# Kernel optimization log

Measured on AMD Instinct MI355X. Metric: run time of the kernel, lower is better.

The kernel has to match this reference:

```python
import jax, jax.numpy as jnp
import numpy as np

B, SQ, SK, D, H = 4, 2048, 2048, 1024, 16
EPS = 1e-6  # flax LayerNorm default


def layer_norm(x, g, b):
    m = x.mean(-1, keepdims=True)
    var = ((x - m) ** 2).mean(-1, keepdims=True)
    return (x - m) * jax.lax.rsqrt(var + EPS) * g + b


def setup_inputs() -> dict:
    key = jax.random.key(0)
    ks = jax.random.split(key, 16)
    s = 1.0 / np.sqrt(D).astype(np.float32)
    inp = {
        'q': jax.random.normal(ks[0], (B, SQ, D), jnp.float32),
        'k': jax.random.normal(ks[1], (B, SK, D), jnp.float32),
        'v': jax.random.normal(ks[2], (B, SK, D), jnp.float32),
        'mask': jax.random.randint(ks[3], (B, SK), 0, 2).astype(bool),
        'Wq': jax.random.normal(ks[4], (D, D), jnp.float32) * s,
        'bq': jnp.zeros((D,), jnp.float32),
        'Wk': jax.random.normal(ks[5], (D, D), jnp.float32) * s,
        'bk': jnp.zeros((D,), jnp.float32),
        'Wv': jax.random.normal(ks[6], (D, D), jnp.float32) * s,
        'bv': jnp.zeros((D,), jnp.float32),
        'Wo': jax.random.normal(ks[7], (D, D), jnp.float32) * s,
        'bo': jnp.zeros((D,), jnp.float32),
        'g1': jnp.ones((D,), jnp.float32),
        'b1': jnp.zeros((D,), jnp.float32),
        'g2': jnp.ones((D,), jnp.float32),
        'b2': jnp.zeros((D,), jnp.float32),
    }
    return inp


def reference(q, k, v, mask, Wq, bq, Wk, bk, Wv, bv, Wo, bo, g1, b1, g2, b2):
    qp = q @ Wq + bq                      # [B, SQ, D]
    kp = k @ Wk + bk                      # [B, SK, D]
    vp = v @ Wv + bv
    qh = qp.reshape(B, SQ, H, D // H)     # head = slice of last dim (matches scatter)
    kh = kp.reshape(B, SK, H, D // H)
    vh = vp.reshape(B, SK, H, D // H)
    # NOTE: original scales by sqrt(dim_out) (full dim), not head dim
    logits = jnp.einsum('bqhd,bkhd->bhqk', qh, kh) / np.sqrt(D).astype(np.float32)
    m = mask[:, None, None, :]            # [B,1,1,SK] broadcast over heads & queries
    A = jax.nn.softmax(jnp.where(m, logits, -jnp.inf), axis=-1)
    A = jnp.where(jnp.isnan(A), 0.0, A)   # fully-masked rows -> 0 (as in original)
    attn = jnp.einsum('bhqk,bkhd->bqhd', A, vh).reshape(B, SQ, D)  # gather heads
    x = layer_norm(qp + attn, g1, b1)
    out = layer_norm(x + jax.nn.relu(x @ Wo + bo), g2, b2)
    return out
```

## Files before the change

kernel.cpp:

```cpp
#include <hip/hip_runtime.h>

#define B_   4
#define SQS  2048
#define SKS  2048
#define DM   1024
#define H_   16
#define MT   8192

typedef __attribute__((ext_vector_type(8))) short bf16x8;
typedef __attribute__((ext_vector_type(4))) float f32x4;

__device__ __forceinline__ float bf2f(unsigned int u) { return __uint_as_float(u << 16); }
__device__ __forceinline__ unsigned short f2bf(float f) {
  unsigned int u = __float_as_uint(f);
  return (unsigned short)((u + 0x7fffu + ((u >> 16) & 1u)) >> 16);
}
__device__ __forceinline__ unsigned int pk_bf16(float a, float b) {
  return __builtin_amdgcn_perm(__float_as_uint(b) + 0x8000u,
                               __float_as_uint(a) + 0x8000u, 0x07060302u);
}
__device__ __forceinline__ unsigned int pk_trunc(float a, float b) {
  return __builtin_amdgcn_perm(__float_as_uint(b), __float_as_uint(a), 0x07060302u);
}
__device__ __forceinline__ float fexp2(float x) {
#if __has_builtin(__builtin_amdgcn_exp2f)
  return __builtin_amdgcn_exp2f(x);
#else
  return __expf(x * 0.69314718056f);
#endif
}
__device__ __forceinline__ void async16(const void* g, void* l) {
  __builtin_amdgcn_global_load_lds((const __attribute__((address_space(1))) unsigned int*)g,
                                   (__attribute__((address_space(3))) unsigned int*)l,
                                   16, 0, 0);
}

#define KSCALE 0.0450842200f
#define BIAS_UNMASKED 0.0028151213f

__global__ __launch_bounds__(256)
void prep_all(const float* __restrict__ q, const float* __restrict__ k,
              const float* __restrict__ v, const int* __restrict__ mask,
              const float* __restrict__ Wq, const float* __restrict__ Wk,
              const float* __restrict__ Wv, const float* __restrict__ Wo,
              unsigned short* __restrict__ qi, unsigned short* __restrict__ ki,
              unsigned short* __restrict__ vi,
              unsigned short* __restrict__ Wqt, unsigned short* __restrict__ Wkt,
              unsigned short* __restrict__ Wvt, unsigned short* __restrict__ Wot,
              float* __restrict__ mskb)
{
  __shared__ float s[32][33];
  const int bx = blockIdx.x, tid = threadIdx.x;
  if (bx < 24576) {
    const int which = bx >> 13, i = bx & 8191;
    const float* src = (which == 0) ? q : (which == 1) ? k : v;
    unsigned short* dst = (which == 0) ? qi : (which == 1) ? ki : vi;
    size_t o = ((size_t)i * 256 + tid) * 4;
    float4 f = *(const float4*)(src + o);
    uint2 u;
    u.x = pk_bf16(f.x, f.y);
    u.y = pk_bf16(f.z, f.w);
    *(uint2*)(dst + o) = u;
  } else if (bx < 28672) {
    const int idx = bx - 24576;
    const int w = idx >> 10, t = idx & 1023;
    const int n0 = (t & 31) * 32, k0 = (t >> 5) * 32;
    const float* W = (w == 0) ? Wq : (w == 1) ? Wk : (w == 2) ? Wv : Wo;
    unsigned short* Wt = (w == 0) ? Wqt : (w == 1) ? Wkt : (w == 2) ? Wvt : Wot;
#pragma unroll
    for (int p = 0; p < 4; p++) {
      int c = p * 256 + tid;
      int r = c >> 5, cc = c & 31;
      s[r][cc] = W[(size_t)(k0 + r) * DM + n0 + cc];
    }
    __syncthreads();
#pragma unroll
    for (int p = 0; p < 4; p++) {
      int c = p * 256 + tid;
      int r = c >> 5, cc = c & 31;
      Wt[(size_t)(n0 + r) * DM + k0 + cc] = f2bf(s[cc][r]);
    }
  } else {
    int i = (bx - 28672) * 256 + tid;
    mskb[i] = mask[i] ? BIAS_UNMASKED : -1e30f;
  }
}

__global__ __launch_bounds__(256)
void qkv_gemm(const unsigned short* __restrict__ A0, const unsigned short* __restrict__ A1,
              const unsigned short* __restrict__ A2,
              const unsigned short* __restrict__ W0, const unsigned short* __restrict__ W1,
              const unsigned short* __restrict__ W2,
              const float* __restrict__ s0, const float* __restrict__ s1,
              const float* __restrict__ s2,
              unsigned short* __restrict__ o0, unsigned short* __restrict__ o1,
              unsigned short* __restrict__ vT)
{
  const int L = blockIdx.x + (blockIdx.y << 3) + (blockIdx.z << 9);
  const int g = L & 7, i5 = L >> 3;
  const int nblk = i5 & 7;
  const int yz = (i5 >> 3) + g * 24;
  const int mblk = yz & 63;
  const int z = yz >> 6;

  const unsigned short* A  = (z == 0) ? A0 : (z == 1) ? A1 : A2;
  const unsigned short* Wt = (z == 0) ? W0 : (z == 1) ? W1 : W2;
  const float* bias        = (z == 0) ? s0 : (z == 1) ? s1 : s2;

  __shared__ short As[128 * 64];
  __shared__ short Bs[128 * 64];
  const int tid = threadIdx.x;
  const int m0 = mblk * 128, n0 = nblk * 128;
  const int wave = tid >> 6, ln = tid & 15, qd = (tid & 63) >> 4;
  const int wm = (wave >> 1) * 64, wn = (wave & 1) * 64;

  int srow[4], sgj[4];
#pragma unroll
  for (int u = 0; u < 4; u++) {
    int c = u * 256 + tid;
    srow[u] = c >> 3;
    sgj[u] = ((c & 7) ^ (srow[u] & 7)) * 8;
  }

  f32x4 acc[4][4];
  const f32x4 vzero = {0.f, 0.f, 0.f, 0.f};
#pragma unroll
  for (int i = 0; i < 4; i++)
#pragma unroll
    for (int j = 0; j < 4; j++) acc[i][j] = vzero;

  for (int k0 = 0; k0 < DM; k0 += 64) {
    __syncthreads();
#pragma unroll
    for (int u = 0; u < 4; u++) {
      int c = u * 256 + tid;
      async16(A  + (size_t)(m0 + srow[u]) * DM + k0 + sgj[u], (char*)As + c * 16);
      async16(Wt + (size_t)(n0 + srow[u]) * DM + k0 + sgj[u], (char*)Bs + c * 16);
    }
    __syncthreads();

#pragma unroll
    for (int kk = 0; kk < 2; kk++) {
      const int ch = ((kk * 4 + qd) ^ (ln & 7)) * 8;
      bf16x8 af[4], bfr[4];
#pragma unroll
      for (int i = 0; i < 4; i++)
        af[i] = *(const bf16x8*)(As + (wm + i * 16 + ln) * 64 + ch);
#pragma unroll
      for (int j = 0; j < 4; j++)
        bfr[j] = *(const bf16x8*)(Bs + (wn + j * 16 + ln) * 64 + ch);
#pragma unroll
      for (int i = 0; i < 4; i++)
#pragma unroll
        for (int j = 0; j < 4; j++)
          acc[i][j] = __builtin_amdgcn_mfma_f32_16x16x32_bf16(af[i], bfr[j], acc[i][j], 0, 0, 0);
    }
  }

  if (z != 2) {
    unsigned short* C = (z == 0) ? o0 : o1;
    const float sc = (z == 1) ? KSCALE : 1.0f;
#pragma unroll
    for (int j = 0; j < 4; j++) {
      int col = n0 + wn + j * 16 + ln;
      float bj = bias[col];
#pragma unroll
      for (int i = 0; i < 4; i++) {
        int row = m0 + wm + i * 16 + qd * 4;
#pragma unroll
        for (int r = 0; r < 4; r++)
          C[(size_t)(row + r) * DM + col] = f2bf((acc[i][j][r] + bj) * sc);
      }
    }
  } else {
#pragma unroll
    for (int j = 0; j < 4; j++) {
      int col = n0 + wn + j * 16 + ln;
      int h = col >> 6, d = col & 63;
      float bj = bias[col];
#pragma unroll
      for (int i = 0; i < 4; i++) {
        int tok0 = m0 + wm + i * 16 + qd * 4;
        int bb = tok0 >> 11;
        int kcol = ((tok0 & 2047) & ~63) + (i & 1) * 32 + qd * 8 + ((i >> 1) & 1) * 4;
        uint2 u;
        u.x = pk_bf16(acc[i][j][0] + bj, acc[i][j][1] + bj);
        u.y = pk_bf16(acc[i][j][2] + bj, acc[i][j][3] + bj);
        *(uint2*)(vT + ((size_t)(bb * H_ + h) * 64 + d) * SKS + kcol) = u;
      }
    }
  }
}

__global__ __launch_bounds__(256)
void gemm_bf16(const unsigned short* __restrict__ A,
               const unsigned short* __restrict__ Wt,
               const float* __restrict__ bias,
               unsigned short* __restrict__ C,
               int relu)
{
  const int L = blockIdx.x + (blockIdx.y << 3);
  const int g = L & 7, i5 = L >> 3;
  const int nblk = i5 & 7;
  const int mblk = (i5 >> 3) + (g << 3);

  __shared__ short As[128 * 64];
  __shared__ short Bs[128 * 64];
  const int tid = threadIdx.x;
  const int m0 = mblk * 128, n0 = nblk * 128;
  const int wave = tid >> 6, ln = tid & 15, qd = (tid & 63) >> 4;
  const int wm = (wave >> 1) * 64, wn = (wave & 1) * 64;

  int srow[4], sgj[4];
#pragma unroll
  for (int u = 0; u < 4; u++) {
    int c = u * 256 + tid;
    srow[u] = c >> 3;
    sgj[u] = ((c & 7) ^ (srow[u] & 7)) * 8;
  }

  f32x4 acc[4][4];
  const f32x4 vzero = {0.f, 0.f, 0.f, 0.f};
#pragma unroll
  for (int i = 0; i < 4; i++)
#pragma unroll
    for (int j = 0; j < 4; j++) acc[i][j] = vzero;

  for (int k0 = 0; k0 < DM; k0 += 64) {
    __syncthreads();
#pragma unroll
    for (int u = 0; u < 4; u++) {
      int c = u * 256 + tid;
      async16(A  + (size_t)(m0 + srow[u]) * DM + k0 + sgj[u], (char*)As + c * 16);
      async16(Wt + (size_t)(n0 + srow[u]) * DM + k0 + sgj[u], (char*)Bs + c * 16);
    }
    __syncthreads();

#pragma unroll
    for (int kk = 0; kk < 2; kk++) {
      const int ch = ((kk * 4 + qd) ^ (ln & 7)) * 8;
      bf16x8 af[4], bfr[4];
#pragma unroll
      for (int i = 0; i < 4; i++)
        af[i] = *(const bf16x8*)(As + (wm + i * 16 + ln) * 64 + ch);
#pragma unroll
      for (int j = 0; j < 4; j++)
        bfr[j] = *(const bf16x8*)(Bs + (wn + j * 16 + ln) * 64 + ch);
#pragma unroll
      for (int i = 0; i < 4; i++)
#pragma unroll
        for (int j = 0; j < 4; j++)
          acc[i][j] = __builtin_amdgcn_mfma_f32_16x16x32_bf16(af[i], bfr[j], acc[i][j], 0, 0, 0);
    }
  }

#pragma unroll
  for (int j = 0; j < 4; j++) {
    int col = n0 + wn + j * 16 + ln;
    float bj = bias[col];
#pragma unroll
    for (int i = 0; i < 4; i++) {
      int row = m0 + wm + i * 16 + qd * 4;
#pragma unroll
      for (int r = 0; r < 4; r++) {
        float v = acc[i][j][r] + bj;
        if (relu) v = fmaxf(v, 0.f);
        C[(size_t)(row + r) * DM + col] = f2bf(v);
      }
    }
  }
}

__global__ __launch_bounds__(256, 2)
void attn_fwd(const unsigned short* __restrict__ qp,
              const unsigned short* __restrict__ kp,
              const unsigned short* __restrict__ vT,
              const float* __restrict__ maskb,
              unsigned short* __restrict__ O0,
              unsigned short* __restrict__ O1,
              float* __restrict__ lws)
{
  __shared__ short Ks[128 * 64];
  __shared__ short Vs[64 * 128];
  __shared__ float bias_s[128];

  const int tid = threadIdx.x;
  const int L = blockIdx.x + (blockIdx.y << 4) + (blockIdx.z << 8);
  const int g = L & 7, i5 = L >> 3;
  const int half = i5 & 1;
  const int qblk = (i5 >> 1) & 7;
  const int bh = (i5 >> 4) + (g << 3);
  const int h = bh & 15, b = bh >> 4;
  const int q0 = qblk * 256;
  const int koff0 = half * (SKS / 2);
  const int wave = tid >> 6, ln = tid & 15, qd = (tid & 63) >> 4;

  int kRow[4], kOff[4], vRow[4], vOff[4];
#pragma unroll
  for (int u = 0; u < 4; u++) {
    int c = u * 256 + tid;
    kRow[u] = c >> 3;
    kOff[u] = ((c & 7) ^ (kRow[u] & 7)) * 8;
    vRow[u] = c >> 4;
    int j = c & 15;
    vOff[u] = ((j & 8) | ((j ^ vRow[u]) & 7)) * 8;
  }

  const unsigned short* kbase = kp + (size_t)(b * SKS) * DM + (h << 6);
  const unsigned short* vbase = vT + (size_t)((b * H_ + h) * 64) * SKS;

  bf16x8 qf[4][2];
#pragma unroll
  for (int gq = 0; gq < 4; gq++) {
    const unsigned short* qrow =
        qp + (size_t)(b * SQS + q0 + wave * 64 + gq * 16 + ln) * DM + (h << 6);
    qf[gq][0] = *(const bf16x8*)(qrow + qd * 8);
    qf[gq][1] = *(const bf16x8*)(qrow + 32 + qd * 8);
  }

  union { bf16x8 v; unsigned int u[4]; } onesf;
  onesf.u[0] = onesf.u[1] = onesf.u[2] = onesf.u[3] = 0x3F803F80u;

  const f32x4 vzero = {0.f, 0.f, 0.f, 0.f};
  f32x4 oA[4][4], lacc[4];
#pragma unroll
  for (int gq = 0; gq < 4; gq++) {
    lacc[gq] = vzero;
#pragma unroll
    for (int t = 0; t < 4; t++) oA[gq][t] = vzero;
  }

  for (int kt = 0; kt < SKS / 2 / 128; kt++) {
    const int k0 = koff0 + kt * 128;
    __syncthreads();
    if (tid < 128) bias_s[tid] = maskb[b * SKS + k0 + tid];
#pragma unroll
    for (int u = 0; u < 4; u++) {
      int c = u * 256 + tid;
      async16(kbase + (size_t)(k0 + kRow[u]) * DM + kOff[u], (char*)Ks + c * 16);
      async16(vbase + (size_t)vRow[u] * SKS + k0 + vOff[u], (char*)Vs + c * 16);
    }
    __syncthreads();

#pragma unroll
    for (int h2 = 0; h2 < 2; h2++) {
      bf16x8 kf[4][2];
      f32x4 btv[4];
#pragma unroll
      for (int t = 0; t < 4; t++) {
        const short* krow = Ks + (h2 * 64 + t * 16 + ln) * 64;
        kf[t][0] = *(const bf16x8*)(krow + ((0 + qd) ^ (ln & 7)) * 8);
        kf[t][1] = *(const bf16x8*)(krow + ((4 + qd) ^ (ln & 7)) * 8);
        btv[t] = *(const f32x4*)(bias_s + h2 * 64 + t * 16 + qd * 4);
      }

      bf16x8 pf[4][2];
#pragma unroll
      for (int gq = 0; gq < 4; gq++) {
        f32x4 sS[4];
#pragma unroll
        for (int t = 0; t < 4; t++) {
          f32x4 a = __builtin_amdgcn_mfma_f32_16x16x32_bf16(kf[t][0], qf[gq][0], btv[t], 0, 0, 0);
          sS[t]   = __builtin_amdgcn_mfma_f32_16x16x32_bf16(kf[t][1], qf[gq][1], a,      0, 0, 0);
        }
        float p[4][4];
#pragma unroll
        for (int t = 0; t < 4; t++) {
          p[t][0] = fexp2(sS[t][0]);
          p[t][1] = fexp2(sS[t][1]);
          p[t][2] = fexp2(sS[t][2]);
          p[t][3] = fexp2(sS[t][3]);
        }
        union { bf16x8 v; unsigned int u[4]; } P0, P1;
        P0.u[0] = pk_trunc(p[0][0], p[0][1]);
        P0.u[1] = pk_trunc(p[0][2], p[0][3]);
        P0.u[2] = pk_trunc(p[2][0], p[2][1]);
        P0.u[3] = pk_trunc(p[2][2], p[2][3]);
        P1.u[0] = pk_trunc(p[1][0], p[1][1]);
        P1.u[1] = pk_trunc(p[1][2], p[1][3]);
        P1.u[2] = pk_trunc(p[3][0], p[3][1]);
        P1.u[3] = pk_trunc(p[3][2], p[3][3]);
        pf[gq][0] = P0.v;
        pf[gq][1] = P1.v;
        lacc[gq] = __builtin_amdgcn_mfma_f32_16x16x32_bf16(pf[gq][0], onesf.v, lacc[gq], 0, 0, 0);
        lacc[gq] = __builtin_amdgcn_mfma_f32_16x16x32_bf16(pf[gq][1], onesf.v, lacc[gq], 0, 0, 0);
      }

#pragma unroll
      for (int t2 = 0; t2 < 4; t2++) {
        const short* vrow = Vs + (t2 * 16 + ln) * 128;
        bf16x8 vf0 = *(const bf16x8*)(vrow + (h2 * 8 + ((0 + qd) ^ (ln & 7))) * 8);
        bf16x8 vf1 = *(const bf16x8*)(vrow + (h2 * 8 + ((4 + qd) ^ (ln & 7))) * 8);
#pragma unroll
        for (int gq = 0; gq < 4; gq++) {
          oA[gq][t2] = __builtin_amdgcn_mfma_f32_16x16x32_bf16(pf[gq][0], vf0, oA[gq][t2], 0, 0, 0);
          oA[gq][t2] = __builtin_amdgcn_mfma_f32_16x16x32_bf16(pf[gq][1], vf1, oA[gq][t2], 0, 0, 0);
        }
      }
    }
  }

  unsigned short* obuf = half ? O1 : O0;
  float* lbuf = lws + (size_t)half * (B_ * H_ * SQS);
#pragma unroll
  for (int gq = 0; gq < 4; gq++) {
    int qloc = q0 + wave * 64 + gq * 16 + qd * 4;
    if (ln == 0) {
#pragma unroll
      for (int r = 0; r < 4; r++)
        lbuf[(size_t)(b * H_ + h) * SQS + qloc + r] = lacc[gq][r];
    }
#pragma unroll
    for (int t2 = 0; t2 < 4; t2++)
#pragma unroll
      for (int r = 0; r < 4; r++) {
        size_t idx = (size_t)(b * SQS + qloc + r) * DM + (h << 6) + t2 * 16 + ln;
        obuf[idx] = f2bf(oA[gq][t2][r]);
      }
  }
}

__global__ __launch_bounds__(256)
void ln_merge(const unsigned short* __restrict__ Xa, const unsigned short* __restrict__ O0,
              const unsigned short* __restrict__ O1, const float* __restrict__ lws,
              const float* __restrict__ gamma, const float* __restrict__ beta,
              unsigned short* __restrict__ outb)
{
  const int row = blockIdx.x, tid = threadIdx.x;
  const int b = row >> 11, q = row & 2047;
  const int h = tid >> 4;
  const size_t lidx = (size_t)(b * H_ + h) * SQS + q;
  float la = lws[lidx], lb2 = lws[lidx + (size_t)(B_ * H_ * SQS)];
  float lsum = la + lb2;
  float linv = (lsum > 0.f) ? 1.0f / lsum : 0.f;

  const size_t base = (size_t)row * DM + tid * 4;
  uint2 ua = *(const uint2*)(Xa + base);
  uint2 u0 = *(const uint2*)(O0 + base);
  uint2 u1 = *(const uint2*)(O1 + base);
  float v0 = bf2f(ua.x & 0xffffu) + (bf2f(u0.x & 0xffffu) + bf2f(u1.x & 0xffffu)) * linv;
  float v1 = bf2f(ua.x >> 16)     + (bf2f(u0.x >> 16)     + bf2f(u1.x >> 16))     * linv;
  float v2 = bf2f(ua.y & 0xffffu) + (bf2f(u0.y & 0xffffu) + bf2f(u1.y & 0xffffu)) * linv;
  float v3 = bf2f(ua.y >> 16)     + (bf2f(u0.y >> 16)     + bf2f(u1.y >> 16))     * linv;

  float s  = (v0 + v1) + (v2 + v3);
  float s2 = (v0 * v0 + v1 * v1) + (v2 * v2 + v3 * v3);
#pragma unroll
  for (int off = 1; off < 64; off <<= 1) {
    s  += __shfl_xor(s, off);
    s2 += __shfl_xor(s2, off);
  }
  __shared__ float red[8];
  if ((tid & 63) == 0) { red[tid >> 6] = s; red[4 + (tid >> 6)] = s2; }
  __syncthreads();
  float S  = (red[0] + red[1]) + (red[2] + red[3]);
  float S2 = (red[4] + red[5]) + (red[6] + red[7]);
  float mean = S * (1.0f / 1024.0f);
  float var  = S2 * (1.0f / 1024.0f) - mean * mean;
  float rstd = rsqrtf(var + 1e-6f);
  int c = tid * 4;
  float o0 = (v0 - mean) * rstd * gamma[c + 0] + beta[c + 0];
  float o1 = (v1 - mean) * rstd * gamma[c + 1] + beta[c + 1];
  float o2 = (v2 - mean) * rstd * gamma[c + 2] + beta[c + 2];
  float o3 = (v3 - mean) * rstd * gamma[c + 3] + beta[c + 3];
  uint2 o;
  o.x = pk_bf16(o0, o1);
  o.y = pk_bf16(o2, o3);
  *(uint2*)(outb + base) = o;
}

__global__ __launch_bounds__(256)
void ln_fuse(const unsigned short* __restrict__ Xa, const unsigned short* __restrict__ Xb,
             const float* __restrict__ gamma, const float* __restrict__ beta,
             float* __restrict__ outf)
{
  const int row = blockIdx.x, tid = threadIdx.x;
  const size_t base = (size_t)row * DM + tid * 4;
  uint2 ua = *(const uint2*)(Xa + base);
  uint2 ub = *(const uint2*)(Xb + base);
  float v0 = bf2f(ua.x & 0xffffu) + bf2f(ub.x & 0xffffu);
  float v1 = bf2f(ua.x >> 16)     + bf2f(ub.x >> 16);
  float v2 = bf2f(ua.y & 0xffffu) + bf2f(ub.y & 0xffffu);
  float v3 = bf2f(ua.y >> 16)     + bf2f(ub.y >> 16);
  float s  = (v0 + v1) + (v2 + v3);
  float s2 = (v0 * v0 + v1 * v1) + (v2 * v2 + v3 * v3);
#pragma unroll
  for (int off = 1; off < 64; off <<= 1) {
    s  += __shfl_xor(s, off);
    s2 += __shfl_xor(s2, off);
  }
  __shared__ float red[8];
  if ((tid & 63) == 0) { red[tid >> 6] = s; red[4 + (tid >> 6)] = s2; }
  __syncthreads();
  float S  = (red[0] + red[1]) + (red[2] + red[3]);
  float S2 = (red[4] + red[5]) + (red[6] + red[7]);
  float mean = S * (1.0f / 1024.0f);
  float var  = S2 * (1.0f / 1024.0f) - mean * mean;
  float rstd = rsqrtf(var + 1e-6f);
  int c = tid * 4;
  float o0 = (v0 - mean) * rstd * gamma[c + 0] + beta[c + 0];
  float o1 = (v1 - mean) * rstd * gamma[c + 1] + beta[c + 1];
  float o2 = (v2 - mean) * rstd * gamma[c + 2] + beta[c + 2];
  float o3 = (v3 - mean) * rstd * gamma[c + 3] + beta[c + 3];
  float4 o = {o0, o1, o2, o3};
  *(float4*)(outf + base) = o;
}

extern "C" void kernel_launch(void* const* d_in, const int* in_sizes, int n_in,
                              void* d_out, int out_size, void* d_ws, size_t ws_size,
                              hipStream_t stream)
{
  (void)in_sizes; (void)n_in; (void)out_size; (void)ws_size;
  const float* q    = (const float*)d_in[0];
  const float* k    = (const float*)d_in[1];
  const float* v    = (const float*)d_in[2];
  const int*   mask = (const int*)  d_in[3];
  const float* Wq   = (const float*)d_in[4];
  const float* bq   = (const float*)d_in[5];
  const float* Wk   = (const float*)d_in[6];
  const float* bk   = (const float*)d_in[7];
  const float* Wv   = (const float*)d_in[8];
  const float* bv   = (const float*)d_in[9];
  const float* Wo   = (const float*)d_in[10];
  const float* bo   = (const float*)d_in[11];
  const float* g1   = (const float*)d_in[12];
  const float* b1   = (const float*)d_in[13];
  const float* g2   = (const float*)d_in[14];
  const float* b2   = (const float*)d_in[15];

  char* ws = (char*)d_ws;
  const size_t SZ16 = (size_t)16 << 20;
  unsigned short* qi   = (unsigned short*)(ws + 0 * SZ16);
  unsigned short* ki   = (unsigned short*)(ws + 1 * SZ16);
  unsigned short* vi   = (unsigned short*)(ws + 2 * SZ16);
  unsigned short* qpb  = (unsigned short*)(ws + 3 * SZ16);
  unsigned short* kpb  = (unsigned short*)(ws + 4 * SZ16);
  unsigned short* vTb  = (unsigned short*)(ws + 6 * SZ16);
  unsigned short* Wqt  = (unsigned short*)(ws + 7 * SZ16 + ((size_t)0 << 20));
  unsigned short* Wkt  = (unsigned short*)(ws + 7 * SZ16 + ((size_t)2 << 20));
  unsigned short* Wvt  = (unsigned short*)(ws + 7 * SZ16 + ((size_t)4 << 20));
  unsigned short* Wot  = (unsigned short*)(ws + 7 * SZ16 + ((size_t)6 << 20));
  float*          mskb = (float*)         (ws + 7 * SZ16 + ((size_t)8 << 20));
  float*          lws  = (float*)         (ws + 7 * SZ16 + ((size_t)9 << 20));
  unsigned short* O0b  = qi;
  unsigned short* O1b  = vi;
  unsigned short* xb   = ki;
  unsigned short* hb   = vTb;

  prep_all     <<<28704,            256, 0, stream>>>(q, k, v, mask, Wq, Wk, Wv, Wo,
                                                      qi, ki, vi, Wqt, Wkt, Wvt, Wot, mskb);

  qkv_gemm     <<<dim3(8, 64, 3),   256, 0, stream>>>(qi, ki, vi, Wqt, Wkt, Wvt,
                                                      bq, bk, bv, qpb, kpb, vTb);

  attn_fwd     <<<dim3(16, 16, 4),  256, 0, stream>>>(qpb, kpb, vTb, mskb, O0b, O1b, lws);

  ln_merge     <<<8192,             256, 0, stream>>>(qpb, O0b, O1b, lws, g1, b1, xb);
  gemm_bf16    <<<dim3(8, 64),      256, 0, stream>>>(xb, Wot, bo, hb, 1);
  ln_fuse      <<<8192,             256, 0, stream>>>(xb, hb, g2, b2, (float*)d_out);
}
```

Measured before the change: 346.9 us.

## Double-buffer K/V tiles in attention kernel with async prefetch and setprio

The attention kernel moves from a single 128-key shared tile to two 64-key buffers. The next tile is prefetched asynchronously while the current one is computed, so the global-load latency is meant to overlap with the MFMA work. The mask bias for the whole key half is loaded once up front instead of every iteration, and s_setprio raises wave priority around the MFMA sections. This costs one __syncthreads per smaller tile and relies on async16 completing before the barrier; there is no explicit wait on the load counter, which is a correctness risk.

```diff
diff --git a/kernel.cpp b/kernel.cpp
--- a/kernel.cpp
+++ b/kernel.cpp
@@ -280,9 +280,9 @@
               unsigned short* __restrict__ O1,
               float* __restrict__ lws)
 {
-  __shared__ short Ks[128 * 64];
-  __shared__ short Vs[64 * 128];
-  __shared__ float bias_s[128];
+  __shared__ __align__(16) short Ks[2][64 * 64];
+  __shared__ __align__(16) short Vs[2][64 * 64];
+  __shared__ __align__(16) float bias_all[1024];
 
   const int tid = threadIdx.x;
   const int L = blockIdx.x + (blockIdx.y << 4) + (blockIdx.z << 8);
@@ -295,19 +295,18 @@
   const int koff0 = half * (SKS / 2);
   const int wave = tid >> 6, ln = tid & 15, qd = (tid & 63) >> 4;
 
-  int kRow[4], kOff[4], vRow[4], vOff[4];
-#pragma unroll
-  for (int u = 0; u < 4; u++) {
+  int sRow[2], sOff[2];
+#pragma unroll
+  for (int u = 0; u < 2; u++) {
     int c = u * 256 + tid;
-    kRow[u] = c >> 3;
-    kOff[u] = ((c & 7) ^ (kRow[u] & 7)) * 8;
-    vRow[u] = c >> 4;
-    int j = c & 15;
-    vOff[u] = ((j & 8) | ((j ^ vRow[u]) & 7)) * 8;
+    sRow[u] = c >> 3;
+    sOff[u] = ((c & 7) ^ (sRow[u] & 7)) * 8;
   }
 
   const unsigned short* kbase = kp + (size_t)(b * SKS) * DM + (h << 6);
   const unsigned short* vbase = vT + (size_t)((b * H_ + h) * 64) * SKS;
+
+  *(float4*)(bias_all + tid * 4) = *(const float4*)(maskb + b * SKS + koff0 + tid * 4);
 
   bf16x8 qf[4][2];
 #pragma unroll
@@ -330,74 +329,88 @@
     for (int t = 0; t < 4; t++) oA[gq][t] = vzero;
   }
 
-  for (int kt = 0; kt < SKS / 2 / 128; kt++) {
-    const int k0 = koff0 + kt * 128;
+#pragma unroll
+  for (int u = 0; u < 2; u++) {
+    int c = u * 256 + tid;
+    async16(kbase + (size_t)(koff0 + sRow[u]) * DM + sOff[u], (char*)Ks[0] + c * 16);
+    async16(vbase + (size_t)sRow[u] * SKS + koff0 + sOff[u], (char*)Vs[0] + c * 16);
+  }
+  __syncthreads();
+
+  const int NT = SKS / 2 / 64;
+  for (int kt = 0; kt < NT; kt++) {
+    const int cur = kt & 1;
+    if (kt + 1 < NT) {
+      const int k1 = koff0 + (kt + 1) * 64;
+#pragma unroll
+      for (int u = 0; u < 2; u++) {
+        int c = u * 256 + tid;
+        async16(kbase + (size_t)(k1 + sRow[u]) * DM + sOff[u], (char*)Ks[cur ^ 1] + c * 16);
+        async16(vbase + (size_t)sRow[u] * SKS + k1 + sOff[u], (char*)Vs[cur ^ 1] + c * 16);
+      }
+    }
+    const short* Ksb = Ks[cur];
+    const short* Vsb = Vs[cur];
+
+    bf16x8 kf[4][2];
+    f32x4 btv[4];
+#pragma unroll
+    for (int t = 0; t < 4; t++) {
+      const short* krow = Ksb + (t * 16 + ln) * 64;
+      kf[t][0] = *(const bf16x8*)(krow + ((0 + qd) ^ (ln & 7)) * 8);
+      kf[t][1] = *(const bf16x8*)(krow + ((4 + qd) ^ (ln & 7)) * 8);
+      btv[t] = *(const f32x4*)(bias_all + kt * 64 + t * 16 + qd * 4);
+    }
+
+    bf16x8 pf[4][2];
+#pragma unroll
+    for (int gq = 0; gq < 4; gq++) {
+      f32x4 sS[4];
+      __builtin_amdgcn_s_setprio(1);
+#pragma unroll
+      for (int t = 0; t < 4; t++) {
+        f32x4 a = __builtin_amdgcn_mfma_f32_16x16x32_bf16(kf[t][0], qf[gq][0], btv[t], 0, 0, 0);
+        sS[t]   = __builtin_amdgcn_mfma_f32_16x16x32_bf16(kf[t][1], qf[gq][1], a,      0, 0, 0);
+      }
+      __builtin_amdgcn_s_setprio(0);
+      float p[4][4];
+#pragma unroll
+      for (int t = 0; t < 4; t++) {
+        p[t][0] = fexp2(sS[t][0]);
+        p[t][1] = fexp2(sS[t][1]);
+        p[t][2] = fexp2(sS[t][2]);
+        p[t][3] = fexp2(sS[t][3]);
+      }
+      union { bf16x8 v; unsigned int u[4]; } P0, P1;
+      P0.u[0] = pk_trunc(p[0][0], p[0][1]);
+      P0.u[1] = pk_trunc(p[0][2], p[0][3]);
+      P0.u[2] = pk_trunc(p[2][0], p[2][1]);
+      P0.u[3] = pk_trunc(p[2][2], p[2][3]);
+      P1.u[0] = pk_trunc(p[1][0], p[1][1]);
+      P1.u[1] = pk_trunc(p[1][2], p[1][3]);
+      P1.u[2] = pk_trunc(p[3][0], p[3][1]);
+      P1.u[3] = pk_trunc(p[3][2], p[3][3]);
+      pf[gq][0] = P0.v;
+      pf[gq][1] = P1.v;
+      lacc[gq] = __builtin_amdgcn_mfma_f32_16x16x32_bf16(pf[gq][0], onesf.v, lacc[gq], 0, 0, 0);
+      lacc[gq] = __builtin_amdgcn_mfma_f32_16x16x32_bf16(pf[gq][1], onesf.v, lacc[gq], 0, 0, 0);
+    }
+
+    __builtin_amdgcn_s_setprio(1);
+#pragma unroll
+    for (int t2 = 0; t2 < 4; t2++) {
+      const short* vrow = Vsb + (t2 * 16 + ln) * 64;
+      bf16x8 vf0 = *(const bf16x8*)(vrow + (((0 + qd) ^ (ln & 7))) * 8);
+      bf16x8 vf1 = *(const bf16x8*)(vrow + (((4 + qd) ^ (ln & 7))) * 8);
+#pragma unroll
+      for (int gq = 0; gq < 4; gq++) {
+        oA[gq][t2] = __builtin_amdgcn_mfma_f32_16x16x32_bf16(pf[gq][0], vf0, oA[gq][t2], 0, 0, 0);
+        oA[gq][t2] = __builtin_amdgcn_mfma_f32_16x16x32_bf16(pf[gq][1], vf1, oA[gq][t2], 0, 0, 0);
+      }
+    }
+    __builtin_amdgcn_s_setprio(0);
+
     __syncthreads();
-    if (tid < 128) bias_s[tid] = maskb[b * SKS + k0 + tid];
-#pragma unroll
-    for (int u = 0; u < 4; u++) {
-      int c = u * 256 + tid;
-      async16(kbase + (size_t)(k0 + kRow[u]) * DM + kOff[u], (char*)Ks + c * 16);
-      async16(vbase + (size_t)vRow[u] * SKS + k0 + vOff[u], (char*)Vs + c * 16);
-    }
-    __syncthreads();
-
-#pragma unroll
-    for (int h2 = 0; h2 < 2; h2++) {
-      bf16x8 kf[4][2];
-      f32x4 btv[4];
-#pragma unroll
-      for (int t = 0; t < 4; t++) {
-        const short* krow = Ks + (h2 * 64 + t * 16 + ln) * 64;
-        kf[t][0] = *(const bf16x8*)(krow + ((0 + qd) ^ (ln & 7)) * 8);
-        kf[t][1] = *(const bf16x8*)(krow + ((4 + qd) ^ (ln & 7)) * 8);
-        btv[t] = *(const f32x4*)(bias_s + h2 * 64 + t * 16 + qd * 4);
-      }
-
-      bf16x8 pf[4][2];
-#pragma unroll
-      for (int gq = 0; gq < 4; gq++) {
-        f32x4 sS[4];
-#pragma unroll
-        for (int t = 0; t < 4; t++) {
-          f32x4 a = __builtin_amdgcn_mfma_f32_16x16x32_bf16(kf[t][0], qf[gq][0], btv[t], 0, 0, 0);
-          sS[t]   = __builtin_amdgcn_mfma_f32_16x16x32_bf16(kf[t][1], qf[gq][1], a,      0, 0, 0);
-        }
-        float p[4][4];
-#pragma unroll
-        for (int t = 0; t < 4; t++) {
-          p[t][0] = fexp2(sS[t][0]);
-          p[t][1] = fexp2(sS[t][1]);
-          p[t][2] = fexp2(sS[t][2]);
-          p[t][3] = fexp2(sS[t][3]);
-        }
-        union { bf16x8 v; unsigned int u[4]; } P0, P1;
-        P0.u[0] = pk_trunc(p[0][0], p[0][1]);
-        P0.u[1] = pk_trunc(p[0][2], p[0][3]);
-        P0.u[2] = pk_trunc(p[2][0], p[2][1]);
-        P0.u[3] = pk_trunc(p[2][2], p[2][3]);
-        P1.u[0] = pk_trunc(p[1][0], p[1][1]);
-        P1.u[1] = pk_trunc(p[1][2], p[1][3]);
-        P1.u[2] = pk_trunc(p[3][0], p[3][1]);
-        P1.u[3] = pk_trunc(p[3][2], p[3][3]);
-        pf[gq][0] = P0.v;
-        pf[gq][1] = P1.v;
-        lacc[gq] = __builtin_amdgcn_mfma_f32_16x16x32_bf16(pf[gq][0], onesf.v, lacc[gq], 0, 0, 0);
-        lacc[gq] = __builtin_amdgcn_mfma_f32_16x16x32_bf16(pf[gq][1], onesf.v, lacc[gq], 0, 0, 0);
-      }
-
-#pragma unroll
-      for (int t2 = 0; t2 < 4; t2++) {
-        const short* vrow = Vs + (t2 * 16 + ln) * 128;
-        bf16x8 vf0 = *(const bf16x8*)(vrow + (h2 * 8 + ((0 + qd) ^ (ln & 7))) * 8);
-        bf16x8 vf1 = *(const bf16x8*)(vrow + (h2 * 8 + ((4 + qd) ^ (ln & 7))) * 8);
-#pragma unroll
-        for (int gq = 0; gq < 4; gq++) {
-          oA[gq][t2] = __builtin_amdgcn_mfma_f32_16x16x32_bf16(pf[gq][0], vf0, oA[gq][t2], 0, 0, 0);
-          oA[gq][t2] = __builtin_amdgcn_mfma_f32_16x16x32_bf16(pf[gq][1], vf1, oA[gq][t2], 0, 0, 0);
-        }
-      }
-    }
   }
 
   unsigned short* obuf = half ? O1 : O0;
```

Measured after the change: 356.2 us. +2.7%, slower.
